# Kernel tuning notes

Measured on AMD Instinct MI355X. Metric: run time of the kernel, lower is better.

Reference implementation:

```python
import jax, jax.numpy as jnp
import numpy as np
from jax import lax

B, C, H, W = 256, 7, 128, 128   # batch, num_bands, img_size, img_size
HID = 256                        # scorer hidden width
SEL = 3                          # selected_bands


def setup_inputs() -> dict:
    key = jax.random.key(0)
    k = jax.random.split(key, 7)
    n = H * W
    x = jax.random.normal(k[0], (B, C, H, W), dtype=jnp.float32)
    # to_qkv: Linear(num_bands, 3*num_bands); stored (in, out) for x @ w. Dead code
    # in the original forward (attn_output unused) but kept for parameter parity.
    w_qkv = jax.random.normal(k[1], (C, 3 * C), dtype=jnp.float32) * (1.0 / np.sqrt(C))
    b_qkv = jnp.zeros((3 * C,), dtype=jnp.float32)
    # band_score_proj: Linear(n, 256) -> ReLU -> Linear(256, 1)
    w1 = jax.random.normal(k[2], (n, HID), dtype=jnp.float32) * (1.0 / np.sqrt(n))
    b1 = jax.random.normal(k[3], (HID,), dtype=jnp.float32) * 0.01
    w2 = jax.random.normal(k[4], (HID, 1), dtype=jnp.float32) * (1.0 / np.sqrt(HID))
    b2 = jax.random.normal(k[5], (1,), dtype=jnp.float32) * 0.01
    return {"x": x, "w_qkv": w_qkv, "b_qkv": b_qkv, "w1": w1, "b1": b1, "w2": w2, "b2": b2}


def reference(x, w_qkv, b_qkv, w1, b1, w2, b2):
    b, c, h, w = x.shape
    feat = x.reshape(b, c, h * w)                  # b c n  (== x_flat.transpose(1,2))
    # NOTE: the original also runs a 1-dim-per-head SDPA on x_flat whose result
    # (attn_output) is never used in the returned values; it is omitted here.
    hid = jax.nn.relu(jnp.einsum('bcn,nk->bck', feat, w1) + b1)   # b c 256
    band_scores = (jnp.einsum('bck,ko->bco', hid, w2) + b2)[..., 0]  # b c
    _, top_indices = lax.top_k(band_scores, SEL)                  # b sel
    selected = jnp.take_along_axis(x, top_indices[:, :, None, None], axis=1)  # b sel h w
    return selected, top_indices
```

## Files before the change

### kernel.cpp

```cpp
#include <hip/hip_runtime.h>

#define Bn    256
#define Cc    7
#define Nn    16384
#define HIDW  256
#define SEL   3
#define Mrows (Bn * Cc)
#define KSPLIT 16
#define KCHUNK (Nn / KSPLIT)
#define BK    32
#define PART_STRIDE ((size_t)Mrows * HIDW)

typedef __attribute__((ext_vector_type(8))) short bf16x8;
typedef __attribute__((ext_vector_type(4))) float floatx4;

#if __has_builtin(__builtin_amdgcn_global_load_lds)
#define HAS_GLDS 1
#endif

__device__ __forceinline__ unsigned pack_hi16(unsigned ua, unsigned ub) {
#if __has_builtin(__builtin_amdgcn_perm)
    return __builtin_amdgcn_perm(ub, ua, 0x07060302u);
#else
    return (ua >> 16) | (ub & 0xffff0000u);
#endif
}

__device__ __forceinline__ void split2(float a, float b, unsigned& hp, unsigned& lp) {
    unsigned ua = __float_as_uint(a), ub = __float_as_uint(b);
    float fa = __uint_as_float(ua & 0xffff0000u);
    float fb = __uint_as_float(ub & 0xffff0000u);
    float la = a - fa, lb = b - fb;
    hp = pack_hi16(ua, ub);
    lp = pack_hi16(__float_as_uint(la), __float_as_uint(lb));
}

__global__ __launch_bounds__(256) void convert_w1(const float* __restrict__ w1,
                                                  unsigned short* __restrict__ bhi,
                                                  unsigned short* __restrict__ blo) {
    const int id = blockIdx.x * 256 + threadIdx.x;
    const int l  = id & 63;
    const int ct = id >> 6;
    const int T  = ct & 15;
    const int c  = ct >> 4;
    const int n  = T * 16 + (l & 15);
    const int k  = c * 32 + (l >> 4) * 8;
    float f[8];
#pragma unroll
    for (int j = 0; j < 8; ++j) f[j] = w1[(size_t)(k + j) * HIDW + n];
    unsigned hp[4], lp[4];
#pragma unroll
    for (int m = 0; m < 4; ++m) split2(f[2 * m], f[2 * m + 1], hp[m], lp[m]);
    *(uint4*)(bhi + (size_t)id * 8) = make_uint4(hp[0], hp[1], hp[2], hp[3]);
    *(uint4*)(blo + (size_t)id * 8) = make_uint4(lp[0], lp[1], lp[2], lp[3]);
}

__global__ __launch_bounds__(256) void gemm_mfma(const float* __restrict__ A,
                                                 const unsigned short* __restrict__ Bhi,
                                                 const unsigned short* __restrict__ Blo,
                                                 float* __restrict__ part) {
    __shared__ unsigned short Ah[4096], Al[4096], Bh[4096], Bl[4096];

    const int bx = blockIdx.x;
    const int m0 = blockIdx.y * 128;
    const int s  = blockIdx.z;
    const int k0 = s * KCHUNK;
    const int t  = threadIdx.x;
    const int lane = t & 63;
    const int w    = t >> 6;
    const int wm   = w & 1;
    const int wn   = w >> 1;

    const int ar  = t >> 1;
    const int kof = (t & 1) * 16;
    const float* aptr = A + (size_t)(m0 + ar) * Nn + k0 + kof;
    const int aidx0 = (ar >> 4) * 512 + ((ar & 15) + ((kof >> 3) + 0) * 16) * 8;
    const int aidx1 = (ar >> 4) * 512 + ((ar & 15) + ((kof >> 3) + 1) * 16) * 8;
    const int wbase = (t & 192) * 8;

    floatx4 acc[4][4];
#pragma unroll
    for (int i = 0; i < 4; ++i)
#pragma unroll
        for (int j = 0; j < 4; ++j) acc[i][j] = (floatx4)0.0f;

    for (int kk = 0; kk < KCHUNK; kk += BK) {
        float4 a0 = *(const float4*)(aptr + kk + 0);
        float4 a1 = *(const float4*)(aptr + kk + 4);
        float4 a2 = *(const float4*)(aptr + kk + 8);
        float4 a3 = *(const float4*)(aptr + kk + 12);
        const size_t bbase = ((size_t)(((k0 + kk) >> 5) * 16 + bx * 8)) * 512;

#ifndef HAS_GLDS
        uint4 bh0 = *(const uint4*)(Bhi + bbase + t * 8);
        uint4 bh1 = *(const uint4*)(Bhi + bbase + 2048 + t * 8);
        uint4 bl0 = *(const uint4*)(Blo + bbase + t * 8);
        uint4 bl1 = *(const uint4*)(Blo + bbase + 2048 + t * 8);
#endif
        float af[16] = {a0.x, a0.y, a0.z, a0.w, a1.x, a1.y, a1.z, a1.w,
                        a2.x, a2.y, a2.z, a2.w, a3.x, a3.y, a3.z, a3.w};
        unsigned hp[8], lp[8];
#pragma unroll
        for (int m = 0; m < 8; ++m) split2(af[2 * m], af[2 * m + 1], hp[m], lp[m]);

        __syncthreads();
#ifdef HAS_GLDS
        __builtin_amdgcn_global_load_lds(
            (const __attribute__((address_space(1))) void*)(Bhi + bbase + t * 8),
            (__attribute__((address_space(3))) void*)&Bh[wbase], 16, 0, 0);
        __builtin_amdgcn_global_load_lds(
            (const __attribute__((address_space(1))) void*)(Bhi + bbase + 2048 + t * 8),
            (__attribute__((address_space(3))) void*)&Bh[2048 + wbase], 16, 0, 0);
        __builtin_amdgcn_global_load_lds(
            (const __attribute__((address_space(1))) void*)(Blo + bbase + t * 8),
            (__attribute__((address_space(3))) void*)&Bl[wbase], 16, 0, 0);
        __builtin_amdgcn_global_load_lds(
            (const __attribute__((address_space(1))) void*)(Blo + bbase + 2048 + t * 8),
            (__attribute__((address_space(3))) void*)&Bl[2048 + wbase], 16, 0, 0);
#else
        *(uint4*)&Bh[t * 8]        = bh0;
        *(uint4*)&Bh[2048 + t * 8] = bh1;
        *(uint4*)&Bl[t * 8]        = bl0;
        *(uint4*)&Bl[2048 + t * 8] = bl1;
#endif
        *(uint4*)&Ah[aidx0] = make_uint4(hp[0], hp[1], hp[2], hp[3]);
        *(uint4*)&Ah[aidx1] = make_uint4(hp[4], hp[5], hp[6], hp[7]);
        *(uint4*)&Al[aidx0] = make_uint4(lp[0], lp[1], lp[2], lp[3]);
        *(uint4*)&Al[aidx1] = make_uint4(lp[4], lp[5], lp[6], lp[7]);
        __syncthreads();

        bf16x8 fah[4], fal[4], fbh[4], fbl[4];
#pragma unroll
        for (int i = 0; i < 4; ++i) {
            fah[i] = *(const bf16x8*)&Ah[(wm * 4 + i) * 512 + lane * 8];
            fal[i] = *(const bf16x8*)&Al[(wm * 4 + i) * 512 + lane * 8];
        }
#pragma unroll
        for (int j = 0; j < 4; ++j) {
            fbh[j] = *(const bf16x8*)&Bh[(wn * 4 + j) * 512 + lane * 8];
            fbl[j] = *(const bf16x8*)&Bl[(wn * 4 + j) * 512 + lane * 8];
        }
#pragma unroll
        for (int i = 0; i < 4; ++i)
#pragma unroll
            for (int j = 0; j < 4; ++j) {
                acc[i][j] = __builtin_amdgcn_mfma_f32_16x16x32_bf16(fah[i], fbh[j], acc[i][j], 0, 0, 0);
                acc[i][j] = __builtin_amdgcn_mfma_f32_16x16x32_bf16(fah[i], fbl[j], acc[i][j], 0, 0, 0);
                acc[i][j] = __builtin_amdgcn_mfma_f32_16x16x32_bf16(fal[i], fbh[j], acc[i][j], 0, 0, 0);
            }
    }

    const int row4 = (lane >> 4) * 4;
    const int col  = lane & 15;
    float* base = part + (size_t)s * PART_STRIDE;
#pragma unroll
    for (int i = 0; i < 4; ++i)
#pragma unroll
        for (int j = 0; j < 4; ++j) {
            const int n = bx * 128 + wn * 64 + j * 16 + col;
#pragma unroll
            for (int p = 0; p < 4; ++p) {
                const int m = m0 + wm * 64 + i * 16 + row4 + p;
                base[(size_t)m * HIDW + n] = acc[i][j][p];
            }
        }
}

__global__ __launch_bounds__(256) void score_rows(const float* __restrict__ part,
                                                  const float* __restrict__ b1,
                                                  const float* __restrict__ w2,
                                                  float* __restrict__ scores) {
    const int r = blockIdx.x;
    const int t = threadIdx.x;
    const size_t off = (size_t)r * HIDW + t;
    float h = 0.0f;
#pragma unroll
    for (int s = 0; s < KSPLIT; ++s) h += part[(size_t)s * PART_STRIDE + off];
    float p = fmaxf(h + b1[t], 0.0f) * w2[t];
#pragma unroll
    for (int o = 32; o > 0; o >>= 1) p += __shfl_down(p, o, 64);
    __shared__ float red[4];
    if ((t & 63) == 0) red[t >> 6] = p;
    __syncthreads();
    if (t == 0) scores[r] = red[0] + red[1] + red[2] + red[3];
}

__global__ __launch_bounds__(256) void topk_kernel(const float* __restrict__ scores,
                                                   float* __restrict__ out,
                                                   int* __restrict__ sidx) {
    const int b = threadIdx.x;
    float sc[Cc];
#pragma unroll
    for (int c = 0; c < Cc; ++c) sc[c] = scores[b * Cc + c];
    bool used[Cc] = {};
#pragma unroll
    for (int k = 0; k < SEL; ++k) {
        int best = 0;
        float bv = -3.4e38f;
#pragma unroll
        for (int c = 0; c < Cc; ++c)
            if (!used[c] && sc[c] > bv) { bv = sc[c]; best = c; }
        used[best] = true;
        sidx[b * SEL + k] = best;
        out[(size_t)Bn * SEL * Nn + b * SEL + k] = (float)best;
    }
}

__global__ __launch_bounds__(256) void gather_bands(const float* __restrict__ x,
                                                    const int* __restrict__ sidx,
                                                    float* __restrict__ out) {
    const int id = blockIdx.x;
    const int b  = id / SEL;
    const int band = sidx[id];
    const float4* src = (const float4*)(x + (size_t)(b * Cc + band) * Nn);
    float4* dst = (float4*)(out + (size_t)id * Nn);
    for (int i = threadIdx.x; i < Nn / 4; i += 256) dst[i] = src[i];
}

extern "C" void kernel_launch(void* const* d_in, const int* in_sizes, int n_in,
                              void* d_out, int out_size, void* d_ws, size_t ws_size,
                              hipStream_t stream) {
    const float* x  = (const float*)d_in[0];
    const float* w1 = (const float*)d_in[3];
    const float* b1 = (const float*)d_in[4];
    const float* w2 = (const float*)d_in[5];
    const float* b2 = (const float*)d_in[6];
    (void)b2;
    float* out = (float*)d_out;

    char* ws = (char*)d_ws;
    float* part = (float*)ws;
    unsigned short* bhi = (unsigned short*)(ws + KSPLIT * PART_STRIDE * sizeof(float));
    unsigned short* blo = bhi + (size_t)Nn * HIDW;
    int*   sidx   = (int*)(blo + (size_t)Nn * HIDW);
    float* scores = (float*)(sidx + Bn * SEL);

    convert_w1<<<(Nn / 32) * 16 * 64 / 256, 256, 0, stream>>>(w1, bhi, blo);
    gemm_mfma<<<dim3(HIDW / 128, Mrows / 128, KSPLIT), 256, 0, stream>>>(x, bhi, blo, part);
    score_rows<<<Mrows, 256, 0, stream>>>(part, b1, w2, scores);
    topk_kernel<<<1, 256, 0, stream>>>(scores, out, sidx);
    gather_bands<<<Bn * SEL, 256, 0, stream>>>(x, sidx, out);
}
```

Before: 263.9 us.

## Double-buffer W1 tiles, load A fragments directly, halve M tile with swizzled grid

Restructures the split-K MFMA GEMM. W1 hi/lo tiles are double-buffered in LDS and prefetched one iteration ahead with async global-to-LDS loads and a partial vmcnt wait. A is no longer staged through LDS; each lane loads its own fp32 fragment into registers, prefetches the next one, and splits it to bf16 hi/lo there. The M tile is halved to 64 rows, giving twice as many workgroups on a 1-D grid with an XCD-oriented swizzle. The aim is to hide global-load latency and cut LDS traffic and barriers, at the cost of less reuse of each B tile per workgroup and reliance on hand-tuned waitcnt correctness.

```diff
diff --git a/kernel.cpp b/kernel.cpp
--- a/kernel.cpp
+++ b/kernel.cpp
@@ -9,13 +9,34 @@
 #define KSPLIT 16
 #define KCHUNK (Nn / KSPLIT)
 #define BK    32
+#define NIT   (KCHUNK / BK)
 #define PART_STRIDE ((size_t)Mrows * HIDW)
 
 typedef __attribute__((ext_vector_type(8))) short bf16x8;
 typedef __attribute__((ext_vector_type(4))) float floatx4;
+typedef __attribute__((ext_vector_type(4))) unsigned int uint32x4;
 
 #if __has_builtin(__builtin_amdgcn_global_load_lds)
 #define HAS_GLDS 1
+#endif
+
+#if __has_builtin(__builtin_amdgcn_sched_barrier)
+#define SCHED_FENCE() __builtin_amdgcn_sched_barrier(0)
+#else
+#define SCHED_FENCE()
+#endif
+
+#ifdef HAS_GLDS
+#define TILE_BARRIER() do { \
+    asm volatile("s_waitcnt vmcnt(4)" ::: "memory"); \
+    __builtin_amdgcn_s_barrier(); \
+    SCHED_FENCE(); \
+} while (0)
+#define GLDS16(src, dst) __builtin_amdgcn_global_load_lds( \
+    (const __attribute__((address_space(1))) void*)(src), \
+    (__attribute__((address_space(3))) void*)(dst), 16, 0, 0)
+#else
+#define TILE_BARRIER() __syncthreads()
 #endif
 
 __device__ __forceinline__ unsigned pack_hi16(unsigned ua, unsigned ub) {
@@ -33,6 +54,22 @@
     float la = a - fa, lb = b - fb;
     hp = pack_hi16(ua, ub);
     lp = pack_hi16(__float_as_uint(la), __float_as_uint(lb));
+}
+
+__device__ __forceinline__ bf16x8 mk_bf16x8(unsigned a, unsigned b, unsigned c, unsigned d) {
+    uint32x4 u = {a, b, c, d};
+    return __builtin_bit_cast(bf16x8, u);
+}
+
+__device__ __forceinline__ void split_frag(const float4& x, const float4& y,
+                                           bf16x8& hi, bf16x8& lo) {
+    unsigned h0, h1, h2, h3, l0, l1, l2, l3;
+    split2(x.x, x.y, h0, l0);
+    split2(x.z, x.w, h1, l1);
+    split2(y.x, y.y, h2, l2);
+    split2(y.z, y.w, h3, l3);
+    hi = mk_bf16x8(h0, h1, h2, h3);
+    lo = mk_bf16x8(l0, l1, l2, l3);
 }
 
 __global__ __launch_bounds__(256) void convert_w1(const float* __restrict__ w1,
@@ -59,94 +96,119 @@
                                                  const unsigned short* __restrict__ Bhi,
                                                  const unsigned short* __restrict__ Blo,
                                                  float* __restrict__ part) {
-    __shared__ unsigned short Ah[4096], Al[4096], Bh[4096], Bl[4096];
-
-    const int bx = blockIdx.x;
-    const int m0 = blockIdx.y * 128;
-    const int s  = blockIdx.z;
-    const int k0 = s * KCHUNK;
-    const int t  = threadIdx.x;
+    __shared__ unsigned short Bh[8192], Bl[8192];
+
+    const int wg  = blockIdx.x;
+    const int swz = (wg & 7) * 112 + (wg >> 3);
+    const int y     = swz % 28;
+    const int combo = swz / 28;
+    const int bx = combo >> 4;
+    const int s  = combo & 15;
+
+    const int m0 = y * 64;
+    const int c0 = s * (KCHUNK / 32);
+    const int t    = threadIdx.x;
     const int lane = t & 63;
     const int w    = t >> 6;
     const int wm   = w & 1;
     const int wn   = w >> 1;
 
-    const int ar  = t >> 1;
-    const int kof = (t & 1) * 16;
-    const float* aptr = A + (size_t)(m0 + ar) * Nn + k0 + kof;
-    const int aidx0 = (ar >> 4) * 512 + ((ar & 15) + ((kof >> 3) + 0) * 16) * 8;
-    const int aidx1 = (ar >> 4) * 512 + ((ar & 15) + ((kof >> 3) + 1) * 16) * 8;
+    const float* aptr0 = A + (size_t)(m0 + wm * 32 + (lane & 15)) * Nn
+                           + (size_t)s * KCHUNK + (lane >> 4) * 8;
+    const float* aptr1 = aptr0 + (size_t)16 * Nn;
+
     const int wbase = (t & 192) * 8;
 
-    floatx4 acc[4][4];
-#pragma unroll
-    for (int i = 0; i < 4; ++i)
+    floatx4 acc[2][4];
+#pragma unroll
+    for (int i = 0; i < 2; ++i)
 #pragma unroll
         for (int j = 0; j < 4; ++j) acc[i][j] = (floatx4)0.0f;
 
-    for (int kk = 0; kk < KCHUNK; kk += BK) {
-        float4 a0 = *(const float4*)(aptr + kk + 0);
-        float4 a1 = *(const float4*)(aptr + kk + 4);
-        float4 a2 = *(const float4*)(aptr + kk + 8);
-        float4 a3 = *(const float4*)(aptr + kk + 12);
-        const size_t bbase = ((size_t)(((k0 + kk) >> 5) * 16 + bx * 8)) * 512;
-
-#ifndef HAS_GLDS
-        uint4 bh0 = *(const uint4*)(Bhi + bbase + t * 8);
-        uint4 bh1 = *(const uint4*)(Bhi + bbase + 2048 + t * 8);
-        uint4 bl0 = *(const uint4*)(Blo + bbase + t * 8);
-        uint4 bl1 = *(const uint4*)(Blo + bbase + 2048 + t * 8);
-#endif
-        float af[16] = {a0.x, a0.y, a0.z, a0.w, a1.x, a1.y, a1.z, a1.w,
-                        a2.x, a2.y, a2.z, a2.w, a3.x, a3.y, a3.z, a3.w};
-        unsigned hp[8], lp[8];
-#pragma unroll
-        for (int m = 0; m < 8; ++m) split2(af[2 * m], af[2 * m + 1], hp[m], lp[m]);
-
-        __syncthreads();
+    {
+        const size_t bb = ((size_t)c0 * 16 + bx * 8) * 512;
 #ifdef HAS_GLDS
-        __builtin_amdgcn_global_load_lds(
-            (const __attribute__((address_space(1))) void*)(Bhi + bbase + t * 8),
-            (__attribute__((address_space(3))) void*)&Bh[wbase], 16, 0, 0);
-        __builtin_amdgcn_global_load_lds(
-            (const __attribute__((address_space(1))) void*)(Bhi + bbase + 2048 + t * 8),
-            (__attribute__((address_space(3))) void*)&Bh[2048 + wbase], 16, 0, 0);
-        __builtin_amdgcn_global_load_lds(
-            (const __attribute__((address_space(1))) void*)(Blo + bbase + t * 8),
-            (__attribute__((address_space(3))) void*)&Bl[wbase], 16, 0, 0);
-        __builtin_amdgcn_global_load_lds(
-            (const __attribute__((address_space(1))) void*)(Blo + bbase + 2048 + t * 8),
-            (__attribute__((address_space(3))) void*)&Bl[2048 + wbase], 16, 0, 0);
-#else
-        *(uint4*)&Bh[t * 8]        = bh0;
-        *(uint4*)&Bh[2048 + t * 8] = bh1;
-        *(uint4*)&Bl[t * 8]        = bl0;
-        *(uint4*)&Bl[2048 + t * 8] = bl1;
-#endif
-        *(uint4*)&Ah[aidx0] = make_uint4(hp[0], hp[1], hp[2], hp[3]);
-        *(uint4*)&Ah[aidx1] = make_uint4(hp[4], hp[5], hp[6], hp[7]);
-        *(uint4*)&Al[aidx0] = make_uint4(lp[0], lp[1], lp[2], lp[3]);
-        *(uint4*)&Al[aidx1] = make_uint4(lp[4], lp[5], lp[6], lp[7]);
-        __syncthreads();
-
-        bf16x8 fah[4], fal[4], fbh[4], fbl[4];
-#pragma unroll
-        for (int i = 0; i < 4; ++i) {
-            fah[i] = *(const bf16x8*)&Ah[(wm * 4 + i) * 512 + lane * 8];
-            fal[i] = *(const bf16x8*)&Al[(wm * 4 + i) * 512 + lane * 8];
+        GLDS16(Bhi + bb + t * 8,        &Bh[wbase]);
+        GLDS16(Bhi + bb + 2048 + t * 8, &Bh[2048 + wbase]);
+        GLDS16(Blo + bb + t * 8,        &Bl[wbase]);
+        GLDS16(Blo + bb + 2048 + t * 8, &Bl[2048 + wbase]);
+#else
+        *(uint4*)&Bh[t * 8]        = *(const uint4*)(Bhi + bb + t * 8);
+        *(uint4*)&Bh[2048 + t * 8] = *(const uint4*)(Bhi + bb + 2048 + t * 8);
+        *(uint4*)&Bl[t * 8]        = *(const uint4*)(Blo + bb + t * 8);
+        *(uint4*)&Bl[2048 + t * 8] = *(const uint4*)(Blo + bb + 2048 + t * 8);
+#endif
+        SCHED_FENCE();
+    }
+    float4 pa0 = *(const float4*)(aptr0);
+    float4 pa1 = *(const float4*)(aptr0 + 4);
+    float4 pa2 = *(const float4*)(aptr1);
+    float4 pa3 = *(const float4*)(aptr1 + 4);
+    TILE_BARRIER();
+
+#pragma unroll 2
+    for (int kk = 0; kk < NIT - 1; ++kk) {
+        const int p = kk & 1;
+        {
+            const size_t bb = ((size_t)(c0 + kk + 1) * 16 + bx * 8) * 512;
+            const int db = (p ^ 1) * 4096 + wbase;
+#ifdef HAS_GLDS
+            GLDS16(Bhi + bb + t * 8,        &Bh[db]);
+            GLDS16(Bhi + bb + 2048 + t * 8, &Bh[db + 2048]);
+            GLDS16(Blo + bb + t * 8,        &Bl[db]);
+            GLDS16(Blo + bb + 2048 + t * 8, &Bl[db + 2048]);
+#else
+            const int ds = (p ^ 1) * 4096;
+            *(uint4*)&Bh[ds + t * 8]        = *(const uint4*)(Bhi + bb + t * 8);
+            *(uint4*)&Bh[ds + 2048 + t * 8] = *(const uint4*)(Bhi + bb + 2048 + t * 8);
+            *(uint4*)&Bl[ds + t * 8]        = *(const uint4*)(Blo + bb + t * 8);
+            *(uint4*)&Bl[ds + 2048 + t * 8] = *(const uint4*)(Blo + bb + 2048 + t * 8);
+#endif
+            SCHED_FENCE();
         }
+        float4 na0 = *(const float4*)(aptr0 + (kk + 1) * BK);
+        float4 na1 = *(const float4*)(aptr0 + (kk + 1) * BK + 4);
+        float4 na2 = *(const float4*)(aptr1 + (kk + 1) * BK);
+        float4 na3 = *(const float4*)(aptr1 + (kk + 1) * BK + 4);
+        bf16x8 ah[2], al[2];
+        split_frag(pa0, pa1, ah[0], al[0]);
+        split_frag(pa2, pa3, ah[1], al[1]);
+        pa0 = na0; pa1 = na1; pa2 = na2; pa3 = na3;
+        bf16x8 fbh[4], fbl[4];
 #pragma unroll
         for (int j = 0; j < 4; ++j) {
-            fbh[j] = *(const bf16x8*)&Bh[(wn * 4 + j) * 512 + lane * 8];
-            fbl[j] = *(const bf16x8*)&Bl[(wn * 4 + j) * 512 + lane * 8];
+            fbh[j] = *(const bf16x8*)&Bh[p * 4096 + (wn * 4 + j) * 512 + lane * 8];
+            fbl[j] = *(const bf16x8*)&Bl[p * 4096 + (wn * 4 + j) * 512 + lane * 8];
         }
 #pragma unroll
-        for (int i = 0; i < 4; ++i)
+        for (int i = 0; i < 2; ++i)
 #pragma unroll
             for (int j = 0; j < 4; ++j) {
-                acc[i][j] = __builtin_amdgcn_mfma_f32_16x16x32_bf16(fah[i], fbh[j], acc[i][j], 0, 0, 0);
-                acc[i][j] = __builtin_amdgcn_mfma_f32_16x16x32_bf16(fah[i], fbl[j], acc[i][j], 0, 0, 0);
-                acc[i][j] = __builtin_amdgcn_mfma_f32_16x16x32_bf16(fal[i], fbh[j], acc[i][j], 0, 0, 0);
+                acc[i][j] = __builtin_amdgcn_mfma_f32_16x16x32_bf16(ah[i], fbh[j], acc[i][j], 0, 0, 0);
+                acc[i][j] = __builtin_amdgcn_mfma_f32_16x16x32_bf16(ah[i], fbl[j], acc[i][j], 0, 0, 0);
+                acc[i][j] = __builtin_amdgcn_mfma_f32_16x16x32_bf16(al[i], fbh[j], acc[i][j], 0, 0, 0);
+            }
+        TILE_BARRIER();
+    }
+
+    {
+        const int p = (NIT - 1) & 1;
+        bf16x8 ah[2], al[2];
+        split_frag(pa0, pa1, ah[0], al[0]);
+        split_frag(pa2, pa3, ah[1], al[1]);
+        bf16x8 fbh[4], fbl[4];
+#pragma unroll
+        for (int j = 0; j < 4; ++j) {
+            fbh[j] = *(const bf16x8*)&Bh[p * 4096 + (wn * 4 + j) * 512 + lane * 8];
+            fbl[j] = *(const bf16x8*)&Bl[p * 4096 + (wn * 4 + j) * 512 + lane * 8];
+        }
+#pragma unroll
+        for (int i = 0; i < 2; ++i)
+#pragma unroll
+            for (int j = 0; j < 4; ++j) {
+                acc[i][j] = __builtin_amdgcn_mfma_f32_16x16x32_bf16(ah[i], fbh[j], acc[i][j], 0, 0, 0);
+                acc[i][j] = __builtin_amdgcn_mfma_f32_16x16x32_bf16(ah[i], fbl[j], acc[i][j], 0, 0, 0);
+                acc[i][j] = __builtin_amdgcn_mfma_f32_16x16x32_bf16(al[i], fbh[j], acc[i][j], 0, 0, 0);
             }
     }
 
@@ -154,14 +216,14 @@
     const int col  = lane & 15;
     float* base = part + (size_t)s * PART_STRIDE;
 #pragma unroll
-    for (int i = 0; i < 4; ++i)
+    for (int i = 0; i < 2; ++i)
 #pragma unroll
         for (int j = 0; j < 4; ++j) {
             const int n = bx * 128 + wn * 64 + j * 16 + col;
 #pragma unroll
-            for (int p = 0; p < 4; ++p) {
-                const int m = m0 + wm * 64 + i * 16 + row4 + p;
-                base[(size_t)m * HIDW + n] = acc[i][j][p];
+            for (int q = 0; q < 4; ++q) {
+                const int m = m0 + wm * 32 + i * 16 + row4 + q;
+                base[(size_t)m * HIDW + n] = acc[i][j][q];
             }
         }
 }
@@ -236,7 +298,7 @@
     float* scores = (float*)(sidx + Bn * SEL);
 
     convert_w1<<<(Nn / 32) * 16 * 64 / 256, 256, 0, stream>>>(w1, bhi, blo);
-    gemm_mfma<<<dim3(HIDW / 128, Mrows / 128, KSPLIT), 256, 0, stream>>>(x, bhi, blo, part);
+    gemm_mfma<<<(HIDW / 128) * (Mrows / 64) * KSPLIT, 256, 0, stream>>>(x, bhi, blo, part);
     score_rows<<<Mrows, 256, 0, stream>>>(part, b1, w2, scores);
     topk_kernel<<<1, 256, 0, stream>>>(scores, out, sidx);
     gather_bands<<<Bn * SEL, 256, 0, stream>>>(x, sidx, out);
```

Result: slower. 293.4 us (+11.2%).

## Prefetch next A tile in GEMM loop and fuse top-k into gather kernel

Applied to the files above, without the earlier changes.

The GEMM main loop now loads the next k-step's A values into registers while the current step's fragments are stored to shared memory. It replaces __syncthreads with raw s_barrier, a manual s_waitcnt vmcnt(4) and sched_barrier fences, so the global-to-LDS B loads can complete while the A prefetch stays in flight. Separately, the single-block top-k kernel is dropped: each gather block recomputes the top-k for its batch row, removing one launch and the sidx round trip. The hand-written waitcnt depends on how many loads the compiler emits, and on the non-GLDS path the count may not cover the B loads correctly.

```diff
diff --git a/kernel.cpp b/kernel.cpp
--- a/kernel.cpp
+++ b/kernel.cpp
@@ -16,6 +16,12 @@
 
 #if __has_builtin(__builtin_amdgcn_global_load_lds)
 #define HAS_GLDS 1
+#endif
+
+#if __has_builtin(__builtin_amdgcn_sched_barrier)
+#define SCHED_FENCE() __builtin_amdgcn_sched_barrier(0)
+#else
+#define SCHED_FENCE()
 #endif
 
 __device__ __forceinline__ unsigned pack_hi16(unsigned ua, unsigned ub) {
@@ -84,26 +90,23 @@
 #pragma unroll
         for (int j = 0; j < 4; ++j) acc[i][j] = (floatx4)0.0f;
 
+    float4 pa0 = *(const float4*)(aptr + 0);
+    float4 pa1 = *(const float4*)(aptr + 4);
+    float4 pa2 = *(const float4*)(aptr + 8);
+    float4 pa3 = *(const float4*)(aptr + 12);
+
     for (int kk = 0; kk < KCHUNK; kk += BK) {
-        float4 a0 = *(const float4*)(aptr + kk + 0);
-        float4 a1 = *(const float4*)(aptr + kk + 4);
-        float4 a2 = *(const float4*)(aptr + kk + 8);
-        float4 a3 = *(const float4*)(aptr + kk + 12);
+        float af[16] = {pa0.x, pa0.y, pa0.z, pa0.w, pa1.x, pa1.y, pa1.z, pa1.w,
+                        pa2.x, pa2.y, pa2.z, pa2.w, pa3.x, pa3.y, pa3.z, pa3.w};
+        unsigned hp[8], lp[8];
+#pragma unroll
+        for (int m = 0; m < 8; ++m) split2(af[2 * m], af[2 * m + 1], hp[m], lp[m]);
+
+        SCHED_FENCE();
+        __builtin_amdgcn_s_barrier();
+        SCHED_FENCE();
+
         const size_t bbase = ((size_t)(((k0 + kk) >> 5) * 16 + bx * 8)) * 512;
-
-#ifndef HAS_GLDS
-        uint4 bh0 = *(const uint4*)(Bhi + bbase + t * 8);
-        uint4 bh1 = *(const uint4*)(Bhi + bbase + 2048 + t * 8);
-        uint4 bl0 = *(const uint4*)(Blo + bbase + t * 8);
-        uint4 bl1 = *(const uint4*)(Blo + bbase + 2048 + t * 8);
-#endif
-        float af[16] = {a0.x, a0.y, a0.z, a0.w, a1.x, a1.y, a1.z, a1.w,
-                        a2.x, a2.y, a2.z, a2.w, a3.x, a3.y, a3.z, a3.w};
-        unsigned hp[8], lp[8];
-#pragma unroll
-        for (int m = 0; m < 8; ++m) split2(af[2 * m], af[2 * m + 1], hp[m], lp[m]);
-
-        __syncthreads();
 #ifdef HAS_GLDS
         __builtin_amdgcn_global_load_lds(
             (const __attribute__((address_space(1))) void*)(Bhi + bbase + t * 8),
@@ -118,16 +121,31 @@
             (const __attribute__((address_space(1))) void*)(Blo + bbase + 2048 + t * 8),
             (__attribute__((address_space(3))) void*)&Bl[2048 + wbase], 16, 0, 0);
 #else
-        *(uint4*)&Bh[t * 8]        = bh0;
-        *(uint4*)&Bh[2048 + t * 8] = bh1;
-        *(uint4*)&Bl[t * 8]        = bl0;
-        *(uint4*)&Bl[2048 + t * 8] = bl1;
-#endif
+        *(uint4*)&Bh[t * 8]        = *(const uint4*)(Bhi + bbase + t * 8);
+        *(uint4*)&Bh[2048 + t * 8] = *(const uint4*)(Bhi + bbase + 2048 + t * 8);
+        *(uint4*)&Bl[t * 8]        = *(const uint4*)(Blo + bbase + t * 8);
+        *(uint4*)&Bl[2048 + t * 8] = *(const uint4*)(Blo + bbase + 2048 + t * 8);
+#endif
+        SCHED_FENCE();
+
         *(uint4*)&Ah[aidx0] = make_uint4(hp[0], hp[1], hp[2], hp[3]);
         *(uint4*)&Ah[aidx1] = make_uint4(hp[4], hp[5], hp[6], hp[7]);
         *(uint4*)&Al[aidx0] = make_uint4(lp[0], lp[1], lp[2], lp[3]);
         *(uint4*)&Al[aidx1] = make_uint4(lp[4], lp[5], lp[6], lp[7]);
-        __syncthreads();
+        const int kn = (kk + BK < KCHUNK) ? (kk + BK) : kk;
+        pa0 = *(const float4*)(aptr + kn + 0);
+        pa1 = *(const float4*)(aptr + kn + 4);
+        pa2 = *(const float4*)(aptr + kn + 8);
+        pa3 = *(const float4*)(aptr + kn + 12);
+
+        SCHED_FENCE();
+#ifdef HAS_GLDS
+        asm volatile("s_waitcnt vmcnt(4) lgkmcnt(0)" ::: "memory");
+#else
+        asm volatile("s_waitcnt vmcnt(4) lgkmcnt(0)" ::: "memory");
+#endif
+        __builtin_amdgcn_s_barrier();
+        SCHED_FENCE();
 
         bf16x8 fah[4], fal[4], fbh[4], fbl[4];
 #pragma unroll
@@ -185,33 +203,30 @@
     if (t == 0) scores[r] = red[0] + red[1] + red[2] + red[3];
 }
 
-__global__ __launch_bounds__(256) void topk_kernel(const float* __restrict__ scores,
-                                                   float* __restrict__ out,
-                                                   int* __restrict__ sidx) {
-    const int b = threadIdx.x;
+__global__ __launch_bounds__(256) void gather_bands(const float* __restrict__ x,
+                                                    const float* __restrict__ scores,
+                                                    float* __restrict__ out) {
+    const int id = blockIdx.x;
+    const int b  = id / SEL;
+    const int kk = id - b * SEL;
     float sc[Cc];
 #pragma unroll
     for (int c = 0; c < Cc; ++c) sc[c] = scores[b * Cc + c];
     bool used[Cc] = {};
-#pragma unroll
-    for (int k = 0; k < SEL; ++k) {
+    int band = 0;
+#pragma unroll
+    for (int k = 0; k <= SEL - 1; ++k) {
         int best = 0;
         float bv = -3.4e38f;
 #pragma unroll
         for (int c = 0; c < Cc; ++c)
             if (!used[c] && sc[c] > bv) { bv = sc[c]; best = c; }
         used[best] = true;
-        sidx[b * SEL + k] = best;
-        out[(size_t)Bn * SEL * Nn + b * SEL + k] = (float)best;
+        if (k == kk) band = best;
+        if (k > kk) break;
     }
-}
-
-__global__ __launch_bounds__(256) void gather_bands(const float* __restrict__ x,
-                                                    const int* __restrict__ sidx,
-                                                    float* __restrict__ out) {
-    const int id = blockIdx.x;
-    const int b  = id / SEL;
-    const int band = sidx[id];
+    if (threadIdx.x == 0)
+        out[(size_t)Bn * SEL * Nn + b * SEL + kk] = (float)band;
     const float4* src = (const float4*)(x + (size_t)(b * Cc + band) * Nn);
     float4* dst = (float4*)(out + (size_t)id * Nn);
     for (int i = threadIdx.x; i < Nn / 4; i += 256) dst[i] = src[i];
@@ -232,12 +247,10 @@
     float* part = (float*)ws;
     unsigned short* bhi = (unsigned short*)(ws + KSPLIT * PART_STRIDE * sizeof(float));
     unsigned short* blo = bhi + (size_t)Nn * HIDW;
-    int*   sidx   = (int*)(blo + (size_t)Nn * HIDW);
-    float* scores = (float*)(sidx + Bn * SEL);
+    float* scores = (float*)(blo + (size_t)Nn * HIDW);
 
     convert_w1<<<(Nn / 32) * 16 * 64 / 256, 256, 0, stream>>>(w1, bhi, blo);
     gemm_mfma<<<dim3(HIDW / 128, Mrows / 128, KSPLIT), 256, 0, stream>>>(x, bhi, blo, part);
     score_rows<<<Mrows, 256, 0, stream>>>(part, b1, w2, scores);
-    topk_kernel<<<1, 256, 0, stream>>>(scores, out, sidx);
-    gather_bands<<<Bn * SEL, 256, 0, stream>>>(x, sidx, out);
-}
+    gather_bands<<<Bn * SEL, 256, 0, stream>>>(x, scores, out);
+}
```

After: 256.3 us. 2.9% less time.
